# Performance work log

Hardware: AMD Instinct MI355X
Metric: run time of the kernel (lower is better)

## Reference

```python
import jax, jax.numpy as jnp
import numpy as np
from jax import lax

DN = ('NHWC', 'HWIO', 'NHWC')  # conv dimension numbers


def setup_inputs() -> dict:
    key = jax.random.key(0)
    ks = jax.random.split(key, 10)
    B, H, W, C, F, E = 16, 32, 32, 128, 128, 8
    G = F * (H // 2) * (W // 2)  # 32768, gating flatten size
    return {
        'x': jax.random.normal(ks[0], (B, H, W, C), jnp.float32),
        'eps_kernel': jax.random.normal(ks[1], (3, 3, C, F, E), jnp.float32),
        'eps_gate': jax.random.normal(ks[2], (B, E), jnp.float32),
        'expert_mu': jax.random.normal(ks[3], (3, 3, C, F, E), jnp.float32) * 0.05,
        'expert_rho': jax.random.normal(ks[4], (3, C, F, E), jnp.float32) * 0.01 - 6.0,
        'expert_bias': jax.random.normal(ks[5], (F, E), jnp.float32) * 0.01,
        'gating_kernel': jax.random.normal(ks[6], (3, 3, C, F), jnp.float32) * 0.05,
        'gating_bias': jax.random.normal(ks[7], (F,), jnp.float32) * 0.01,
        'gating_out_kernel': jax.random.normal(ks[8], (G, E), jnp.float32) * 0.01,
        'gating_out_bias': jax.random.normal(ks[9], (E,), jnp.float32) * 0.01,
    }


def reference(x, eps_kernel, eps_gate, expert_mu, expert_rho, expert_bias,
              gating_kernel, gating_bias, gating_out_kernel, gating_out_bias):
    GATING_NOISE_SIGMA = 1e-4
    TOP_K = 2
    B = x.shape[0]
    kh, kw, C, F, E = expert_mu.shape

    # Bayesian reparameterized expert kernels: rho shared over first kernel dim
    sigma = jax.nn.softplus(expert_rho)[None]               # [1,kw,C,F,E]
    kernel = expert_mu + sigma * eps_kernel                 # [kh,kw,C,F,E]

    # All-expert conv as one grouped conv via output-channel packing
    kern_flat = kernel.reshape(kh, kw, C, F * E)
    expert_out = lax.conv_general_dilated(x, kern_flat, (1, 1), 'SAME',
                                          dimension_numbers=DN)
    expert_out = expert_out.reshape(B, x.shape[1], x.shape[2], F, E)
    expert_out = expert_out + expert_bias                   # [B,H,W,F,E]

    # Gating path: conv -> 2x2 maxpool -> flatten -> dense -> noisy logits
    g = lax.conv_general_dilated(x, gating_kernel, (1, 1), 'SAME',
                                 dimension_numbers=DN) + gating_bias
    g = lax.reduce_window(g, -jnp.inf, lax.max,
                          (1, 2, 2, 1), (1, 2, 2, 1), 'VALID')
    logits = g.reshape(B, -1) @ gating_out_kernel + gating_out_bias  # [B,E]
    logits = logits + GATING_NOISE_SIGMA * eps_gate

    # noisy top-k gating: softmax over selected experts, zero elsewhere
    top_vals, top_idx = lax.top_k(logits, TOP_K)
    top_w = jax.nn.softmax(top_vals, axis=-1)
    gates = jnp.zeros((B, E), logits.dtype).at[
        jnp.arange(B)[:, None], top_idx].set(top_w)

    # combine experts weighted by gates, broadcast over spatial dims
    out = jnp.einsum('bhwfe,be->bhwf', expert_out, gates)
    return out
```

## Files before the change

kernel.cpp:

```cpp
#include <hip/hip_runtime.h>
#include <cmath>

#define B_ 16
#define H_ 32
#define W_ 32
#define C_ 128
#define F_ 128
#define KSZ (9*C_*F_)
#define NKS 36
#define FRAG_ELE 4096

typedef __bf16 bf16;
typedef __bf16 bf16x4 __attribute__((ext_vector_type(4)));
typedef __bf16 bf16x8 __attribute__((ext_vector_type(8)));
typedef float  f32x4  __attribute__((ext_vector_type(4)));

__device__ __forceinline__ float softplus_f(float v) {
  return log1pf(expf(-fabsf(v))) + fmaxf(v, 0.f);
}

__device__ __forceinline__ void top2_gates_f(const float* lg, float* gl) {
  int i0 = 0;
  #pragma unroll
  for (int e = 1; e < 8; ++e) if (lg[e] > lg[i0]) i0 = e;
  int i1 = (i0 == 0) ? 1 : 0;
  #pragma unroll
  for (int e = 0; e < 8; ++e) if (e != i0 && lg[e] > lg[i1]) i1 = e;
  float m  = fmaxf(lg[i0], lg[i1]);
  float e0 = expf(lg[i0] - m), e1 = expf(lg[i1] - m);
  float s  = e0 + e1;
  #pragma unroll
  for (int e = 0; e < 8; ++e) gl[e] = 0.f;
  gl[i0] = e0 / s; gl[i1] = e1 / s;
}

__device__ __forceinline__ float logit_f(const float* part, const float* gob,
                                         const float* epsg, int bb, int e) {
  float s = 0.f;
  #pragma unroll
  for (int hb = 0; hb < 16; ++hb) s += part[(bb*16 + hb)*8 + e];
  return s + gob[e] + 1e-4f * epsg[bb*8 + e];
}

__device__ __forceinline__ void block_map_f(int bid, int* b, int* hb) {
  *b  = (bid & 7) * 2 + (bid >> 7);
  *hb = (bid >> 3) & 15;
}

template<int NVAR>
__global__ __launch_bounds__(1024, 4) void conv_k(
    const float* __restrict__ x,
    const bf16* __restrict__ Bhi, const bf16* __restrict__ Blo,
    const float* __restrict__ gb,
    const float* __restrict__ Wg,
    const float* __restrict__ part,
    const float* __restrict__ gob,
    const float* __restrict__ epsg,
    const float* __restrict__ ebias,
    float* __restrict__ outv)
{
  int b, hb;
  block_map_f(blockIdx.x, &b, &hb);
  const int t   = threadIdx.x;
  const int l   = t & 63;
  const int wid = t >> 6;
  const int kg  = wid >> 3;
  const int w8  = wid & 7;

  __shared__ bf16 xs[NVAR*4*34*128];
  __shared__ float red[8][8];
  __shared__ float gl8[8];

  for (int v = t; v < 4*34*32; v += 1024) {
    int c4   = v & 31;
    int col  = (v >> 5) % 34;
    int rowi = (v >> 5) / 34;
    int row  = hb*2 - 1 + rowi;
    int w    = col - 1;
    float4 xv = make_float4(0.f, 0.f, 0.f, 0.f);
    if (row >= 0 && row < H_ && w >= 0 && w < W_)
      xv = *(const float4*)&x[((b*H_ + row)*W_ + w)*C_ + c4*4];
    float vv[4] = {xv.x, xv.y, xv.z, xv.w};
    bf16x4 h4, l4;
    #pragma unroll
    for (int j = 0; j < 4; ++j) {
      h4[j] = (bf16)vv[j];
      if (NVAR == 2) l4[j] = (bf16)(vv[j] - (float)h4[j]);
    }
    int base = ((rowi*34 + col)*256 + c4*8) ^ ((col & 7) << 4);
    *(bf16x4*)((char*)xs + base) = h4;
    if (NVAR == 2) *(bf16x4*)((char*)xs + 34816 + base) = l4;
  }
  if (NVAR == 1 && t == 0) {
    float lg[8], gg[8];
    #pragma unroll
    for (int e = 0; e < 8; ++e) lg[e] = logit_f(part, gob, epsg, b, e);
    top2_gates_f(lg, gg);
    #pragma unroll
    for (int e = 0; e < 8; ++e) gl8[e] = gg[e];
  }
  __syncthreads();

  const int mpar = w8 & 1;
  const int nf0  = (w8 >> 1) << 1;
  const int r15  = l & 15;
  const int q    = l >> 4;

  f32x4 acc00 = {0.f,0.f,0.f,0.f}, acc01 = acc00, acc10 = acc00, acc11 = acc00;

  const bf16* Bh = Bhi + (NVAR == 1 ? (size_t)b * KSZ : (size_t)0);
  const size_t bgo = (size_t)(nf0*512 + l*8);

  bf16x8 s0h0,s0h1,s0l0,s0l1, s1h0,s1h1,s1l0,s1l1, s2h0,s2h1,s2l0,s2l1;

#define LOADB(S, KS_) do {                                                  \
    int kk_ = (KS_); if (kk_ > NKS-1) kk_ = NKS-1;                          \
    size_t o_ = bgo + (size_t)kk_ * FRAG_ELE;                               \
    S##h0 = *(const bf16x8*)(Bh + o_);                                      \
    S##h1 = *(const bf16x8*)(Bh + o_ + 512);                                \
    if (NVAR == 2) {                                                        \
      S##l0 = *(const bf16x8*)(Blo + o_);                                   \
      S##l1 = *(const bf16x8*)(Blo + o_ + 512);                             \
    }                                                                       \
  } while (0)

#define MFMA16(a, bb_, c) __builtin_amdgcn_mfma_f32_16x16x32_bf16(a, bb_, c, 0, 0, 0)

#define COMPUTE(S, KS_) do {                                                \
    const int khkw_ = (KS_) >> 2;                                           \
    const int kh_ = khkw_ / 3, kw_ = khkw_ % 3;                             \
    const int c0_ = ((KS_) & 3) << 5;                                       \
    const int col_ = mpar*16 + r15 + kw_;                                   \
    const int off_ = ((kh_*34 + col_)*256 + (c0_ + q*8)*2) ^ ((col_ & 7) << 4); \
    bf16x8 a0_ = *(const bf16x8*)((const char*)xs + off_);                  \
    bf16x8 a1_ = *(const bf16x8*)((const char*)xs + off_ + 8704);           \
    __builtin_amdgcn_s_setprio(1);                                          \
    acc00 = MFMA16(a0_, S##h0, acc00);                                      \
    acc01 = MFMA16(a0_, S##h1, acc01);                                      \
    acc10 = MFMA16(a1_, S##h0, acc10);                                      \
    acc11 = MFMA16(a1_, S##h1, acc11);                                      \
    if (NVAR == 2) {                                                        \
      bf16x8 g0_ = *(const bf16x8*)((const char*)xs + 34816 + off_);        \
      bf16x8 g1_ = *(const bf16x8*)((const char*)xs + 34816 + off_ + 8704); \
      acc00 = MFMA16(g0_, S##h0, acc00);                                    \
      acc01 = MFMA16(g0_, S##h1, acc01);                                    \
      acc10 = MFMA16(g1_, S##h0, acc10);                                    \
      acc11 = MFMA16(g1_, S##h1, acc11);                                    \
      acc00 = MFMA16(a0_, S##l0, acc00);                                    \
      acc01 = MFMA16(a0_, S##l1, acc01);                                    \
      acc10 = MFMA16(a1_, S##l0, acc10);                                    \
      acc11 = MFMA16(a1_, S##l1, acc11);                                    \
    }                                                                       \
    __builtin_amdgcn_s_setprio(0);                                          \
  } while (0)

  const int ks0 = kg * (NKS/2);
  LOADB(s0, ks0); LOADB(s1, ks0+1); LOADB(s2, ks0+2);
  for (int ks = ks0; ks < ks0 + NKS/2; ks += 3) {
    COMPUTE(s0, ks);   LOADB(s0, ks+3);
    COMPUTE(s1, ks+1); LOADB(s1, ks+4);
    COMPUTE(s2, ks+2); LOADB(s2, ks+5);
  }
#undef LOADB
#undef COMPUTE

  __syncthreads();
  float* comb = (float*)xs;
  if (kg == 1) {
    #pragma unroll
    for (int r = 0; r < 4; ++r) {
      comb[(w8*16 + 0  + r)*64 + l] = acc00[r];
      comb[(w8*16 + 4  + r)*64 + l] = acc01[r];
      comb[(w8*16 + 8  + r)*64 + l] = acc10[r];
      comb[(w8*16 + 12 + r)*64 + l] = acc11[r];
    }
  }
  __syncthreads();
  if (kg == 0) {
    #pragma unroll
    for (int r = 0; r < 4; ++r) {
      acc00[r] += comb[(w8*16 + 0  + r)*64 + l];
      acc01[r] += comb[(w8*16 + 4  + r)*64 + l];
      acc10[r] += comb[(w8*16 + 8  + r)*64 + l];
      acc11[r] += comb[(w8*16 + 12 + r)*64 + l];
    }
  }

  if (NVAR == 1) {
    if (kg == 0) {
      const int f0 = nf0*16 + r15;
      float bv0 = 0.f, bv1 = 0.f;
      #pragma unroll
      for (int e = 0; e < 8; ++e) {
        bv0 += gl8[e] * ebias[f0*8 + e];
        bv1 += gl8[e] * ebias[(f0+16)*8 + e];
      }
      #pragma unroll
      for (int mi = 0; mi < 2; ++mi) {
        const int h = hb*2 + mi;
        #pragma unroll
        for (int r = 0; r < 4; ++r) {
          const int wo = mpar*16 + q*4 + r;
          float* o = &outv[((b*H_ + h)*W_ + wo)*F_];
          o[f0]      = (mi ? acc10[r] : acc00[r]) + bv0;
          o[f0 + 16] = (mi ? acc11[r] : acc01[r]) + bv1;
        }
      }
    }
  } else {
    float pr[8] = {0,0,0,0,0,0,0,0};
    if (kg == 0) {
      #pragma unroll
      for (int ni = 0; ni < 2; ++ni) {
        const int f = (nf0 + ni)*16 + r15;
        const float bv = gb[f];
        #pragma unroll
        for (int pp = 0; pp < 2; ++pp) {
          float m0 = ni ? fmaxf(acc01[2*pp], acc01[2*pp+1])
                        : fmaxf(acc00[2*pp], acc00[2*pp+1]);
          float m1 = ni ? fmaxf(acc11[2*pp], acc11[2*pp+1])
                        : fmaxf(acc10[2*pp], acc10[2*pp+1]);
          float pm = fmaxf(m0, m1) + bv;
          const int pw = mpar*8 + q*2 + pp;
          const float* wr = &Wg[(size_t)((hb*16 + pw)*128 + f) * 8];
          float4 wA = *(const float4*)wr;
          float4 wB = *(const float4*)(wr + 4);
          pr[0] += pm*wA.x; pr[1] += pm*wA.y; pr[2] += pm*wA.z; pr[3] += pm*wA.w;
          pr[4] += pm*wB.x; pr[5] += pm*wB.y; pr[6] += pm*wB.z; pr[7] += pm*wB.w;
        }
      }
    }
    #pragma unroll
    for (int o = 32; o > 0; o >>= 1)
      #pragma unroll
      for (int e = 0; e < 8; ++e) pr[e] += __shfl_down(pr[e], o);
    if (l == 0 && kg == 0)
      #pragma unroll
      for (int e = 0; e < 8; ++e) red[w8][e] = pr[e];
    __syncthreads();
    if (t < 8) {
      float s = 0.f;
      #pragma unroll
      for (int w = 0; w < 8; ++w) s += red[w][t];
      outv[(b*16 + hb)*8 + t] = s;
    }
  }
}

__global__ __launch_bounds__(256) void effk_k(
    const float* __restrict__ mu, const float* __restrict__ rho,
    const float* __restrict__ eps,
    const float* __restrict__ part, const float* __restrict__ gob,
    const float* __restrict__ epsg,
    bf16* __restrict__ Bg)
{
  const int ks  = blockIdx.x >> 3;
  const int rem = blockIdx.x & 7;
  const int t   = threadIdx.x;
  const int nf  = (rem & 1)*4 + (t >> 6);
  const int bq  = (rem >> 1) * 4;

  __shared__ float lgs[4][8];
  __shared__ float gl[4][8];
  if (t < 32) lgs[t >> 3][t & 7] = logit_f(part, gob, epsg, bq + (t >> 3), t & 7);
  __syncthreads();
  if (t < 4) top2_gates_f(lgs[t], gl[t]);
  __syncthreads();

  const int l    = t & 63;
  const int khkw = ks >> 2;
  const int kw   = khkw % 3;
  const int f    = nf*16 + (l & 15);
  const int cb   = (ks & 3)*32 + (l >> 4)*8;

  bf16x8 ob[4];
  #pragma unroll
  for (int j = 0; j < 8; ++j) {
    const int c = cb + j;
    const float* mp = &mu [(size_t)((khkw*C_ + c)*F_ + f) * 8];
    const float* ep = &eps[(size_t)((khkw*C_ + c)*F_ + f) * 8];
    const float* rp = &rho[(size_t)((kw  *C_ + c)*F_ + f) * 8];
    float kv[8];
    #pragma unroll
    for (int e = 0; e < 8; ++e)
      kv[e] = mp[e] + softplus_f(rp[e]) * ep[e];
    #pragma unroll
    for (int bb = 0; bb < 4; ++bb) {
      float s = 0.f;
      #pragma unroll
      for (int e = 0; e < 8; ++e) s += gl[bb][e] * kv[e];
      ob[bb][j] = (bf16)s;
    }
  }
  #pragma unroll
  for (int bb = 0; bb < 4; ++bb) {
    size_t o = (size_t)(bq + bb)*KSZ + (size_t)ks*FRAG_ELE + nf*512 + l*8;
    *(bf16x8*)&Bg[o] = ob[bb];
  }
}

__global__ __launch_bounds__(512) void gkconv_k(
    const float* __restrict__ gk, bf16* __restrict__ bgh, bf16* __restrict__ bgl)
{
  __shared__ float tile[32*129];
  const int ks   = blockIdx.x;
  const int khkw = ks >> 2;
  const int cb   = (ks & 3)*32;
  const int t    = threadIdx.x;

  for (int v = t; v < 1024; v += 512) {
    int c  = v >> 5;
    int f4 = (v & 31) * 4;
    float4 val = *(const float4*)&gk[(size_t)(khkw*C_ + cb + c)*F_ + f4];
    float* dst = &tile[c*129 + f4];
    dst[0] = val.x; dst[1] = val.y; dst[2] = val.z; dst[3] = val.w;
  }
  __syncthreads();

  const int nf = t >> 6, l = t & 63;
  const int f  = nf*16 + (l & 15);
  bf16x8 h8, l8;
  #pragma unroll
  for (int j = 0; j < 8; ++j) {
    int c = (l >> 4)*8 + j;
    float v = tile[c*129 + f];
    bf16 h = (bf16)v;
    h8[j] = h;
    l8[j] = (bf16)(v - (float)h);
  }
  *(bf16x8*)&bgh[(size_t)ks*FRAG_ELE + t*8] = h8;
  *(bf16x8*)&bgl[(size_t)ks*FRAG_ELE + t*8] = l8;
}

extern "C" void kernel_launch(void* const* d_in, const int* in_sizes, int n_in,
                              void* d_out, int out_size, void* d_ws, size_t ws_size,
                              hipStream_t stream) {
  const float* x    = (const float*)d_in[0];
  const float* epsk = (const float*)d_in[1];
  const float* epsg = (const float*)d_in[2];
  const float* mu   = (const float*)d_in[3];
  const float* rho  = (const float*)d_in[4];
  const float* ebias= (const float*)d_in[5];
  const float* gk   = (const float*)d_in[6];
  const float* gb   = (const float*)d_in[7];
  const float* gok  = (const float*)d_in[8];
  const float* gob  = (const float*)d_in[9];
  float* out = (float*)d_out;

  char* ws = (char*)d_ws;
  bf16*  bgh  = (bf16*) (ws);
  bf16*  bgl  = (bf16*) (ws + 294912);
  bf16*  bge  = (bf16*) (ws + 589824);
  float* part = (float*)(ws + 5308416);

  gkconv_k<<<NKS, 512, 0, stream>>>(gk, bgh, bgl);
  conv_k<2><<<B_*16, 1024, 0, stream>>>(x, bgh, bgl, gb, gok,
                                        nullptr, nullptr, nullptr, nullptr, part);
  effk_k<<<NKS*8, 256, 0, stream>>>(mu, rho, epsk, part, gob, epsg, bge);
  conv_k<1><<<B_*16, 1024, 0, stream>>>(x, bge, bge, nullptr, nullptr,
                                        part, gob, epsg, ebias, out);
}
```

Measured before the change: 65.49 us.

## Precompute per-expert kernel bank and run top-2 experts directly in conv

Replaces the per-batch gated effective-kernel build (which ran after the gating conv) with a gate-independent bank of all 8 expert kernels in bf16. The gating-weight preparation is merged into the same launch. The final conv then picks the two selected experts per batch, accumulates each into its own set of registers, and combines them with the softmax gate weights afterwards. This takes the effk kernel off the serial path and removes a launch. In exchange, the final conv issues twice the MFMAs and twice the B loads, and uses four extra accumulator vectors.

```diff
diff --git a/kernel.cpp b/kernel.cpp
--- a/kernel.cpp
+++ b/kernel.cpp
@@ -19,21 +19,6 @@
   return log1pf(expf(-fabsf(v))) + fmaxf(v, 0.f);
 }
 
-__device__ __forceinline__ void top2_gates_f(const float* lg, float* gl) {
-  int i0 = 0;
-  #pragma unroll
-  for (int e = 1; e < 8; ++e) if (lg[e] > lg[i0]) i0 = e;
-  int i1 = (i0 == 0) ? 1 : 0;
-  #pragma unroll
-  for (int e = 0; e < 8; ++e) if (e != i0 && lg[e] > lg[i1]) i1 = e;
-  float m  = fmaxf(lg[i0], lg[i1]);
-  float e0 = expf(lg[i0] - m), e1 = expf(lg[i1] - m);
-  float s  = e0 + e1;
-  #pragma unroll
-  for (int e = 0; e < 8; ++e) gl[e] = 0.f;
-  gl[i0] = e0 / s; gl[i1] = e1 / s;
-}
-
 __device__ __forceinline__ float logit_f(const float* part, const float* gob,
                                          const float* epsg, int bb, int e) {
   float s = 0.f;
@@ -47,10 +32,11 @@
   *hb = (bid >> 3) & 15;
 }
 
-template<int NVAR>
+template<int MODE>
 __global__ __launch_bounds__(1024, 4) void conv_k(
     const float* __restrict__ x,
-    const bf16* __restrict__ Bhi, const bf16* __restrict__ Blo,
+    const bf16* __restrict__ Bhi,
+    const bf16* __restrict__ Blo,
     const float* __restrict__ gb,
     const float* __restrict__ Wg,
     const float* __restrict__ part,
@@ -67,9 +53,11 @@
   const int kg  = wid >> 3;
   const int w8  = wid & 7;
 
-  __shared__ bf16 xs[NVAR*4*34*128];
+  __shared__ bf16 xs[MODE*4*34*128];
   __shared__ float red[8][8];
   __shared__ float gl8[8];
+  __shared__ float gw2[2];
+  __shared__ int   eid2[2];
 
   for (int v = t; v < 4*34*32; v += 1024) {
     int c4   = v & 31;
@@ -85,19 +73,30 @@
     #pragma unroll
     for (int j = 0; j < 4; ++j) {
       h4[j] = (bf16)vv[j];
-      if (NVAR == 2) l4[j] = (bf16)(vv[j] - (float)h4[j]);
+      if (MODE == 2) l4[j] = (bf16)(vv[j] - (float)h4[j]);
     }
     int base = ((rowi*34 + col)*256 + c4*8) ^ ((col & 7) << 4);
     *(bf16x4*)((char*)xs + base) = h4;
-    if (NVAR == 2) *(bf16x4*)((char*)xs + 34816 + base) = l4;
-  }
-  if (NVAR == 1 && t == 0) {
-    float lg[8], gg[8];
+    if (MODE == 2) *(bf16x4*)((char*)xs + 34816 + base) = l4;
+  }
+  if (MODE == 1 && t == 0) {
+    float lg[8];
     #pragma unroll
     for (int e = 0; e < 8; ++e) lg[e] = logit_f(part, gob, epsg, b, e);
-    top2_gates_f(lg, gg);
-    #pragma unroll
-    for (int e = 0; e < 8; ++e) gl8[e] = gg[e];
+    int i0 = 0;
+    #pragma unroll
+    for (int e = 1; e < 8; ++e) if (lg[e] > lg[i0]) i0 = e;
+    int i1 = (i0 == 0) ? 1 : 0;
+    #pragma unroll
+    for (int e = 0; e < 8; ++e) if (e != i0 && lg[e] > lg[i1]) i1 = e;
+    float m  = fmaxf(lg[i0], lg[i1]);
+    float e0 = expf(lg[i0] - m), e1 = expf(lg[i1] - m);
+    float s  = e0 + e1;
+    #pragma unroll
+    for (int e = 0; e < 8; ++e) gl8[e] = 0.f;
+    gl8[i0] = e0 / s;  gl8[i1] = e1 / s;
+    eid2[0] = i0;      eid2[1] = i1;
+    gw2[0]  = e0 / s;  gw2[1]  = e1 / s;
   }
   __syncthreads();
 
@@ -107,8 +106,12 @@
   const int q    = l >> 4;
 
   f32x4 acc00 = {0.f,0.f,0.f,0.f}, acc01 = acc00, acc10 = acc00, acc11 = acc00;
-
-  const bf16* Bh = Bhi + (NVAR == 1 ? (size_t)b * KSZ : (size_t)0);
+  f32x4 acd00 = acc00, acd01 = acc00, acd10 = acc00, acd11 = acc00;
+
+  const bf16* B0;
+  const bf16* B1;
+  if (MODE == 1) { B0 = Bhi + (size_t)eid2[0]*KSZ; B1 = Bhi + (size_t)eid2[1]*KSZ; }
+  else           { B0 = Bhi;                       B1 = Blo; }
   const size_t bgo = (size_t)(nf0*512 + l*8);
 
   bf16x8 s0h0,s0h1,s0l0,s0l1, s1h0,s1h1,s1l0,s1l1, s2h0,s2h1,s2l0,s2l1;
@@ -116,12 +119,10 @@
 #define LOADB(S, KS_) do {                                                  \
     int kk_ = (KS_); if (kk_ > NKS-1) kk_ = NKS-1;                          \
     size_t o_ = bgo + (size_t)kk_ * FRAG_ELE;                               \
-    S##h0 = *(const bf16x8*)(Bh + o_);                                      \
-    S##h1 = *(const bf16x8*)(Bh + o_ + 512);                                \
-    if (NVAR == 2) {                                                        \
-      S##l0 = *(const bf16x8*)(Blo + o_);                                   \
-      S##l1 = *(const bf16x8*)(Blo + o_ + 512);                             \
-    }                                                                       \
+    S##h0 = *(const bf16x8*)(B0 + o_);                                      \
+    S##h1 = *(const bf16x8*)(B0 + o_ + 512);                                \
+    S##l0 = *(const bf16x8*)(B1 + o_);                                      \
+    S##l1 = *(const bf16x8*)(B1 + o_ + 512);                                \
   } while (0)
 
 #define MFMA16(a, bb_, c) __builtin_amdgcn_mfma_f32_16x16x32_bf16(a, bb_, c, 0, 0, 0)
@@ -139,7 +140,7 @@
     acc01 = MFMA16(a0_, S##h1, acc01);                                      \
     acc10 = MFMA16(a1_, S##h0, acc10);                                      \
     acc11 = MFMA16(a1_, S##h1, acc11);                                      \
-    if (NVAR == 2) {                                                        \
+    if (MODE == 2) {                                                        \
       bf16x8 g0_ = *(const bf16x8*)((const char*)xs + 34816 + off_);        \
       bf16x8 g1_ = *(const bf16x8*)((const char*)xs + 34816 + off_ + 8704); \
       acc00 = MFMA16(g0_, S##h0, acc00);                                    \
@@ -150,6 +151,11 @@
       acc01 = MFMA16(a0_, S##l1, acc01);                                    \
       acc10 = MFMA16(a1_, S##l0, acc10);                                    \
       acc11 = MFMA16(a1_, S##l1, acc11);                                    \
+    } else {                                                                \
+      acd00 = MFMA16(a0_, S##l0, acd00);                                    \
+      acd01 = MFMA16(a0_, S##l1, acd01);                                    \
+      acd10 = MFMA16(a1_, S##l0, acd10);                                    \
+      acd11 = MFMA16(a1_, S##l1, acd11);                                    \
     }                                                                       \
     __builtin_amdgcn_s_setprio(0);                                          \
   } while (0)
@@ -164,6 +170,17 @@
 #undef LOADB
 #undef COMPUTE
 
+  if (MODE == 1) {
+    const float g0 = gw2[0], g1 = gw2[1];
+    #pragma unroll
+    for (int r = 0; r < 4; ++r) {
+      acc00[r] = g0*acc00[r] + g1*acd00[r];
+      acc01[r] = g0*acc01[r] + g1*acd01[r];
+      acc10[r] = g0*acc10[r] + g1*acd10[r];
+      acc11[r] = g0*acc11[r] + g1*acd11[r];
+    }
+  }
+
   __syncthreads();
   float* comb = (float*)xs;
   if (kg == 1) {
@@ -186,7 +203,7 @@
     }
   }
 
-  if (NVAR == 1) {
+  if (MODE == 1) {
     if (kg == 0) {
       const int f0 = nf0*16 + r15;
       float bv0 = 0.f, bv1 = 0.f;
@@ -247,89 +264,68 @@
   }
 }
 
-__global__ __launch_bounds__(256) void effk_k(
+__global__ __launch_bounds__(256) void prep_k(
     const float* __restrict__ mu, const float* __restrict__ rho,
-    const float* __restrict__ eps,
-    const float* __restrict__ part, const float* __restrict__ gob,
-    const float* __restrict__ epsg,
-    bf16* __restrict__ Bg)
-{
-  const int ks  = blockIdx.x >> 3;
-  const int rem = blockIdx.x & 7;
-  const int t   = threadIdx.x;
-  const int nf  = (rem & 1)*4 + (t >> 6);
-  const int bq  = (rem >> 1) * 4;
-
-  __shared__ float lgs[4][8];
-  __shared__ float gl[4][8];
-  if (t < 32) lgs[t >> 3][t & 7] = logit_f(part, gob, epsg, bq + (t >> 3), t & 7);
-  __syncthreads();
-  if (t < 4) top2_gates_f(lgs[t], gl[t]);
-  __syncthreads();
-
-  const int l    = t & 63;
-  const int khkw = ks >> 2;
-  const int kw   = khkw % 3;
-  const int f    = nf*16 + (l & 15);
-  const int cb   = (ks & 3)*32 + (l >> 4)*8;
-
-  bf16x8 ob[4];
-  #pragma unroll
-  for (int j = 0; j < 8; ++j) {
-    const int c = cb + j;
-    const float* mp = &mu [(size_t)((khkw*C_ + c)*F_ + f) * 8];
-    const float* ep = &eps[(size_t)((khkw*C_ + c)*F_ + f) * 8];
-    const float* rp = &rho[(size_t)((kw  *C_ + c)*F_ + f) * 8];
-    float kv[8];
-    #pragma unroll
-    for (int e = 0; e < 8; ++e)
-      kv[e] = mp[e] + softplus_f(rp[e]) * ep[e];
-    #pragma unroll
-    for (int bb = 0; bb < 4; ++bb) {
-      float s = 0.f;
-      #pragma unroll
-      for (int e = 0; e < 8; ++e) s += gl[bb][e] * kv[e];
-      ob[bb][j] = (bf16)s;
-    }
-  }
-  #pragma unroll
-  for (int bb = 0; bb < 4; ++bb) {
-    size_t o = (size_t)(bq + bb)*KSZ + (size_t)ks*FRAG_ELE + nf*512 + l*8;
-    *(bf16x8*)&Bg[o] = ob[bb];
-  }
-}
-
-__global__ __launch_bounds__(512) void gkconv_k(
-    const float* __restrict__ gk, bf16* __restrict__ bgh, bf16* __restrict__ bgl)
+    const float* __restrict__ eps, const float* __restrict__ gk,
+    bf16* __restrict__ bank, bf16* __restrict__ bgh, bf16* __restrict__ bgl)
 {
   __shared__ float tile[32*129];
-  const int ks   = blockIdx.x;
-  const int khkw = ks >> 2;
-  const int cb   = (ks & 3)*32;
-  const int t    = threadIdx.x;
-
-  for (int v = t; v < 1024; v += 512) {
-    int c  = v >> 5;
-    int f4 = (v & 31) * 4;
-    float4 val = *(const float4*)&gk[(size_t)(khkw*C_ + cb + c)*F_ + f4];
-    float* dst = &tile[c*129 + f4];
-    dst[0] = val.x; dst[1] = val.y; dst[2] = val.z; dst[3] = val.w;
-  }
-  __syncthreads();
-
-  const int nf = t >> 6, l = t & 63;
-  const int f  = nf*16 + (l & 15);
-  bf16x8 h8, l8;
-  #pragma unroll
-  for (int j = 0; j < 8; ++j) {
-    int c = (l >> 4)*8 + j;
-    float v = tile[c*129 + f];
-    bf16 h = (bf16)v;
-    h8[j] = h;
-    l8[j] = (bf16)(v - (float)h);
-  }
-  *(bf16x8*)&bgh[(size_t)ks*FRAG_ELE + t*8] = h8;
-  *(bf16x8*)&bgl[(size_t)ks*FRAG_ELE + t*8] = l8;
+  const int bid = blockIdx.x;
+  const int t   = threadIdx.x;
+
+  if (bid < 2*NKS) {
+    const int ks = bid >> 1;
+    const int nf = (bid & 1)*4 + (t >> 6);
+    const int l  = t & 63;
+    const int khkw = ks >> 2;
+    const int kw   = khkw % 3;
+    const int f    = nf*16 + (l & 15);
+    const int cb   = (ks & 3)*32 + (l >> 4)*8;
+
+    bf16x8 ob[8];
+    #pragma unroll
+    for (int j = 0; j < 8; ++j) {
+      const int c = cb + j;
+      const float* mp = &mu [(size_t)((khkw*C_ + c)*F_ + f) * 8];
+      const float* ep = &eps[(size_t)((khkw*C_ + c)*F_ + f) * 8];
+      const float* rp = &rho[(size_t)((kw  *C_ + c)*F_ + f) * 8];
+      #pragma unroll
+      for (int e = 0; e < 8; ++e)
+        ob[e][j] = (bf16)(mp[e] + softplus_f(rp[e]) * ep[e]);
+    }
+    #pragma unroll
+    for (int e = 0; e < 8; ++e) {
+      size_t o = (size_t)e*KSZ + (size_t)ks*FRAG_ELE + nf*512 + l*8;
+      *(bf16x8*)&bank[o] = ob[e];
+    }
+  } else {
+    const int ks   = bid - 2*NKS;
+    const int khkw = ks >> 2;
+    const int cb   = (ks & 3)*32;
+    for (int v = t; v < 1024; v += 256) {
+      int c  = v >> 5;
+      int f4 = (v & 31) * 4;
+      float4 val = *(const float4*)&gk[(size_t)(khkw*C_ + cb + c)*F_ + f4];
+      float* dst = &tile[c*129 + f4];
+      dst[0] = val.x; dst[1] = val.y; dst[2] = val.z; dst[3] = val.w;
+    }
+    __syncthreads();
+    for (int tt = t; tt < 512; tt += 256) {
+      const int nf = tt >> 6, l = tt & 63;
+      const int f  = nf*16 + (l & 15);
+      bf16x8 h8, l8;
+      #pragma unroll
+      for (int j = 0; j < 8; ++j) {
+        int c = (l >> 4)*8 + j;
+        float v = tile[c*129 + f];
+        bf16 h = (bf16)v;
+        h8[j] = h;
+        l8[j] = (bf16)(v - (float)h);
+      }
+      *(bf16x8*)&bgh[(size_t)ks*FRAG_ELE + tt*8] = h8;
+      *(bf16x8*)&bgl[(size_t)ks*FRAG_ELE + tt*8] = l8;
+    }
+  }
 }
 
 extern "C" void kernel_launch(void* const* d_in, const int* in_sizes, int n_in,
@@ -348,15 +344,14 @@
   float* out = (float*)d_out;
 
   char* ws = (char*)d_ws;
-  bf16*  bgh  = (bf16*) (ws);
-  bf16*  bgl  = (bf16*) (ws + 294912);
-  bf16*  bge  = (bf16*) (ws + 589824);
-  float* part = (float*)(ws + 5308416);
-
-  gkconv_k<<<NKS, 512, 0, stream>>>(gk, bgh, bgl);
+  bf16*  bank = (bf16*) (ws);
+  bf16*  bgh  = (bf16*) (ws + 2359296);
+  bf16*  bgl  = (bf16*) (ws + 2654208);
+  float* part = (float*)(ws + 2949120);
+
+  prep_k<<<3*NKS, 256, 0, stream>>>(mu, rho, epsk, gk, bank, bgh, bgl);
   conv_k<2><<<B_*16, 1024, 0, stream>>>(x, bgh, bgl, gb, gok,
                                         nullptr, nullptr, nullptr, nullptr, part);
-  effk_k<<<NKS*8, 256, 0, stream>>>(mu, rho, epsk, part, gob, epsg, bge);
-  conv_k<1><<<B_*16, 1024, 0, stream>>>(x, bge, bge, nullptr, nullptr,
+  conv_k<1><<<B_*16, 1024, 0, stream>>>(x, bank, nullptr, nullptr, nullptr,
                                         part, gob, epsg, ebias, out);
 }
```

Result: faster. 55.62 us (-15.1%).
